# Performance work log

Measured on AMD Instinct MI355X. Metric: run time of the kernel, lower is better.

The kernel has to match this reference:

```python
import jax, jax.numpy as jnp
import numpy as np

VOCAB = 10000
HID = 256
BATCH = 32
STEPS = 256


def setup_inputs() -> dict:
    key = jax.random.key(0)
    ks = jax.random.split(key, 8)
    X = jax.random.randint(ks[0], (BATCH, STEPS), 0, VOCAB)
    H = jnp.zeros((BATCH, HID), dtype=jnp.float32)
    s = 0.01
    inp = {
        "X": X,
        "H": H,
        "W_xz": jax.random.normal(ks[1], (VOCAB, HID), jnp.float32) * s,
        "W_hz": jax.random.normal(ks[2], (HID, HID), jnp.float32) * s,
        "b_z": jnp.zeros((HID,), jnp.float32),
        "W_xr": jax.random.normal(ks[3], (VOCAB, HID), jnp.float32) * s,
        "W_hr": jax.random.normal(ks[4], (HID, HID), jnp.float32) * s,
        "b_r": jnp.zeros((HID,), jnp.float32),
        "W_xh": jax.random.normal(ks[5], (VOCAB, HID), jnp.float32) * s,
        "W_hh": jax.random.normal(ks[6], (HID, HID), jnp.float32) * s,
        "b_h": jnp.zeros((HID,), jnp.float32),
        "W_hq": jax.random.normal(ks[7], (HID, VOCAB), jnp.float32) * s,
        "b_q": jnp.zeros((VOCAB,), jnp.float32),
    }
    return inp


def reference(X, H, W_xz, W_hz, b_z, W_xr, W_hr, b_r, W_xh, W_hh, b_h, W_hq, b_q):
    # one-hot of X.T -> (steps, batch, vocab) float32
    Xo = jax.nn.one_hot(X.T, VOCAB, dtype=jnp.float32)

    def step(h, x):  # x: (batch, vocab), h: (batch, hid)
        z = jax.nn.sigmoid(x @ W_xz + h @ W_hz + b_z)
        r = jax.nn.sigmoid(x @ W_xr + h @ W_hr + b_r)
        h_tilda = jnp.tanh(x @ W_xh + (r * h) @ W_hh + b_h)
        h_new = z * h + (1.0 - z) * h_tilda
        y = h_new @ W_hq + b_q  # (batch, vocab)
        return h_new, y

    H_final, Ys = jax.lax.scan(step, H, Xo)
    out = Ys.reshape(STEPS * BATCH, VOCAB)  # matches torch.cat(outputs, dim=0)
    return out, (H_final,)
```

## Files before the change

### kernel.cpp

```cpp
#include <hip/hip_runtime.h>
#include <hip/hip_bf16.h>
#include <stdint.h>

#define VOCAB 10000
#define HID   256
#define BATCH 32
#define STEPS 256

typedef __attribute__((ext_vector_type(8))) short short8;
typedef __attribute__((ext_vector_type(4))) float floatx4;

__device__ __forceinline__ float bf2f(unsigned short u) {
    union { unsigned int ui; float f; } v;
    v.ui = ((unsigned int)u) << 16;
    return v.f;
}

__device__ __forceinline__ unsigned short f2bf(float f) {
    union { float f; unsigned int ui; } v;
    v.f = f;
    unsigned int u = v.ui;
    unsigned int r = (u + 0x7FFFu + ((u >> 16) & 1u)) >> 16;
    return (unsigned short)r;
}

#if __has_builtin(__builtin_amdgcn_fdot2_f32_bf16)
typedef __bf16 bf16x2 __attribute__((ext_vector_type(2)));
__device__ __forceinline__ float dot2(unsigned int w, unsigned int h, float acc) {
    union { unsigned int u; bf16x2 v; } a, b;
    a.u = w; b.u = h;
    return __builtin_amdgcn_fdot2_f32_bf16(a.v, b.v, acc, false);
}
#else
__device__ __forceinline__ float dot2(unsigned int w, unsigned int h, float acc) {
    union { unsigned int u; float f; } w0, w1, h0, h1;
    w0.u = w << 16; w1.u = w & 0xFFFF0000u;
    h0.u = h << 16; h1.u = h & 0xFFFF0000u;
    acc = fmaf(w0.f, h0.f, acc);
    acc = fmaf(w1.f, h1.f, acc);
    return acc;
}
#endif

__device__ __forceinline__ float sigmoidf_(float x) {
    return __builtin_amdgcn_rcpf(1.0f + __expf(-x));
}
__device__ __forceinline__ float tanhf_(float x) {
    float e = __expf(2.0f * x);
    return 1.0f - 2.0f * __builtin_amdgcn_rcpf(e + 1.0f);
}

__global__ void prep_w(const float* __restrict__ Wz, const float* __restrict__ Wr,
                       const float* __restrict__ Wh, unsigned short* __restrict__ out) {
    int g = blockIdx.x, k = blockIdx.y, j = threadIdx.x;
    const float* W = (g == 0) ? Wz : (g == 1) ? Wr : Wh;
    float v = W[k * HID + j];
    int p4 = k >> 3, m = k & 7;
    out[(((size_t)g * 32 + p4) * HID + j) * 8 + m] = f2bf(v);
}

__global__ void prep_b(const float* __restrict__ Whq, unsigned short* __restrict__ bfr) {
    int k = blockIdx.y;
    int n = blockIdx.x * 256 + threadIdx.x;
    if (n >= VOCAB) return;
    float v = Whq[(size_t)k * VOCAB + n];
    int nt = n >> 4, l15 = n & 15;
    int kc = k >> 5, kr = k & 31;
    int quad = kr >> 3, jj = kr & 7;
    int lane = quad * 16 + l15;
    bfr[(((size_t)nt * 8 + kc) * 64 + lane) * 8 + jj] = f2bf(v);
}

__global__ __launch_bounds__(512, 1) void gru_rec(
    const int* __restrict__ X, const float* __restrict__ H0,
    const float* __restrict__ Wxz, const float* __restrict__ Wxr,
    const float* __restrict__ Wxh,
    const float* __restrict__ bz, const float* __restrict__ br,
    const float* __restrict__ bh,
    const unsigned short* __restrict__ Wsw,
    unsigned short* __restrict__ hist,
    float* __restrict__ h_final)
{
    const int b = blockIdx.x;
    const int tid = threadIdx.x;
    const bool isA = tid < HID;
    const int j = isA ? tid : tid - HID;

    __shared__ __align__(16) unsigned short hbuf[HID];
    __shared__ __align__(16) unsigned short rhbuf[HID];
    __shared__ float part[HID];
    __shared__ float xrow[2][3][HID];
    __shared__ int Xl[STEPS];

    const uint4* wA = (const uint4*)Wsw + (size_t)(isA ? 0 : 1) * 32 * HID + j;
    const uint4* wH = (const uint4*)Wsw + (size_t)2 * 32 * HID + j;

    float h_my = H0[b * HID + j];
    float bias = isA ? bz[j] : br[j];
    float bhj  = isA ? bh[j] : 0.0f;

    uint4 wreg[32];
    #pragma unroll
    for (int i = 0; i < 32; ++i) wreg[i] = wA[i * HID];

    const int i0 = isA ? 0 : 16;
    uint4 whreg[16];
    #pragma unroll
    for (int i = 0; i < 16; ++i) whreg[i] = wH[(i0 + i) * HID];

    if (isA) { hbuf[j] = f2bf(h_my); Xl[j] = X[b * STEPS + j]; }
    __syncthreads();

    {
        int x0 = Xl[0];
        if (isA) {
            xrow[0][0][j] = Wxz[(size_t)x0 * HID + j];
            xrow[0][2][j] = Wxh[(size_t)x0 * HID + j];
        } else {
            xrow[0][1][j] = Wxr[(size_t)x0 * HID + j];
        }
    }
    __syncthreads();

    float z = 0.0f;

    for (int t = 0; t < STEPS; ++t) {
        const int cur = t & 1, nxt = cur ^ 1;

        const int xn = Xl[(t + 1) & (STEPS - 1)];
        float p0 = 0.f, p1 = 0.f;
        if (isA) {
            p0 = Wxz[(size_t)xn * HID + j];
            p1 = Wxh[(size_t)xn * HID + j];
        } else {
            p0 = Wxr[(size_t)xn * HID + j];
        }

        float acc;
        {
            const uint4* hp = (const uint4*)hbuf;
            float a0 = 0.f, a1 = 0.f, a2 = 0.f, a3 = 0.f;
            #pragma unroll
            for (int i = 0; i < 32; ++i) {
                uint4 hv = hp[i];
                a0 = dot2(wreg[i].x, hv.x, a0);
                a1 = dot2(wreg[i].y, hv.y, a1);
                a2 = dot2(wreg[i].z, hv.z, a2);
                a3 = dot2(wreg[i].w, hv.w, a3);
            }
            acc = (a0 + a1) + (a2 + a3);
        }

        if (isA) {
            z = sigmoidf_(acc + xrow[cur][0][j] + bias);
            xrow[nxt][0][j] = p0;
            xrow[nxt][2][j] = p1;
        } else {
            float r = sigmoidf_(acc + xrow[cur][1][j] + bias);
            rhbuf[j] = f2bf(r * h_my);
            xrow[nxt][1][j] = p0;
        }
        __syncthreads();

        float acch;
        {
            const uint4* rp = (const uint4*)rhbuf;
            float a0 = 0.f, a1 = 0.f, a2 = 0.f, a3 = 0.f;
            #pragma unroll
            for (int i = 0; i < 16; ++i) {
                uint4 hv = rp[i0 + i];
                a0 = dot2(whreg[i].x, hv.x, a0);
                a1 = dot2(whreg[i].y, hv.y, a1);
                a2 = dot2(whreg[i].z, hv.z, a2);
                a3 = dot2(whreg[i].w, hv.w, a3);
            }
            acch = (a0 + a1) + (a2 + a3);
        }
        if (!isA) part[j] = acch;
        __syncthreads();

        if (isA) {
            float hpre = acch + part[j] + xrow[cur][2][j] + bhj;
            float ht = tanhf_(hpre);
            float hn = z * h_my + (1.0f - z) * ht;
            h_my = hn;
            unsigned short hb = f2bf(hn);
            hbuf[j] = hb;
            hist[((size_t)t * BATCH + b) * HID + j] = hb;
        }
        __syncthreads();

        if (!isA) h_my = bf2f(hbuf[j]);
    }

    if (isA) h_final[b * HID + j] = h_my;
}

__global__ __launch_bounds__(256, 2) void proj(
    const unsigned short* __restrict__ Abf,
    const unsigned short* __restrict__ Bfr,
    const float* __restrict__ bq,
    float* __restrict__ C)
{
    const int tid  = threadIdx.x;
    const int wave = tid >> 6;
    const int lane = tid & 63;
    const int l15  = lane & 15;
    const int quad = lane >> 4;

    const int nb = blockIdx.x;
    const int mb = blockIdx.y;
    const int m0 = mb * 128;
    const int nt0 = nb * 16 + wave * 4;

    floatx4 acc[8][4];
    #pragma unroll
    for (int i = 0; i < 8; ++i)
        #pragma unroll
        for (int q = 0; q < 4; ++q)
            acc[i][q] = (floatx4)0.0f;

    int ntc[4];
    #pragma unroll
    for (int q = 0; q < 4; ++q) {
        int nt = nt0 + q;
        ntc[q] = (nt < 625) ? nt : 624;
    }

    for (int kc = 0; kc < 8; ++kc) {
        short8 a[8];
        #pragma unroll
        for (int mt = 0; mt < 8; ++mt) {
            const unsigned short* ap =
                Abf + (size_t)(m0 + mt * 16 + l15) * HID + kc * 32 + quad * 8;
            a[mt] = *(const short8*)ap;
        }
        short8 bfrg[4];
        #pragma unroll
        for (int q = 0; q < 4; ++q) {
            const unsigned short* bp =
                Bfr + ((((size_t)ntc[q] * 8 + kc) * 64) + lane) * 8;
            bfrg[q] = *(const short8*)bp;
        }
        #pragma unroll
        for (int mt = 0; mt < 8; ++mt)
            #pragma unroll
            for (int q = 0; q < 4; ++q)
                acc[mt][q] = __builtin_amdgcn_mfma_f32_16x16x32_bf16(
                    a[mt], bfrg[q], acc[mt][q], 0, 0, 0);
    }

    #pragma unroll
    for (int q = 0; q < 4; ++q) {
        int nt = nt0 + q;
        if (nt >= 625) continue;
        int col = nt * 16 + l15;
        float bqv = bq[col];
        #pragma unroll
        for (int mt = 0; mt < 8; ++mt) {
            int rowb = m0 + mt * 16 + quad * 4;
            #pragma unroll
            for (int r = 0; r < 4; ++r) {
                C[(size_t)(rowb + r) * VOCAB + col] = acc[mt][q][r] + bqv;
            }
        }
    }
}

extern "C" void kernel_launch(void* const* d_in, const int* in_sizes, int n_in,
                              void* d_out, int out_size, void* d_ws, size_t ws_size,
                              hipStream_t stream) {
    const int*   X   = (const int*)  d_in[0];
    const float* H0  = (const float*)d_in[1];
    const float* Wxz = (const float*)d_in[2];
    const float* Whz = (const float*)d_in[3];
    const float* bz  = (const float*)d_in[4];
    const float* Wxr = (const float*)d_in[5];
    const float* Whr = (const float*)d_in[6];
    const float* br  = (const float*)d_in[7];
    const float* Wxh = (const float*)d_in[8];
    const float* Whh = (const float*)d_in[9];
    const float* bh  = (const float*)d_in[10];
    const float* Whq = (const float*)d_in[11];
    const float* bq  = (const float*)d_in[12];

    float* out     = (float*)d_out;
    float* h_final = out + (size_t)STEPS * BATCH * VOCAB;

    unsigned short* wsw  = (unsigned short*)d_ws;
    unsigned short* bfr  = wsw + 196608;
    unsigned short* hist = bfr + 2560000;

    prep_w<<<dim3(3, 256), 256, 0, stream>>>(Whz, Whr, Whh, wsw);
    prep_b<<<dim3(40, 256), 256, 0, stream>>>(Whq, bfr);
    gru_rec<<<BATCH, 512, 0, stream>>>(X, H0, Wxz, Wxr, Wxh, bz, br, bh,
                                       wsw, hist, h_final);
    proj<<<dim3(40, 64), 256, 0, stream>>>(hist, bfr, bq, out);
}
```

Measured before the change: 851.2 us.

## Vectorize weight prep and projection stores, remap proj blocks per XCD

The weight-prep kernels now pack eight bf16 values per thread and store them as one 16-byte write. prep_b stages a tile of W_hq through LDS to get a transposed layout, so global reads and writes are both coalesced. The projection swaps the MFMA operand order so each lane holds four consecutive output columns and can write 16-byte float4 stores with a float4 bias load. Blocks are also remapped so each XCD handles a contiguous group of N-tiles, which should improve L2 reuse of the B fragments. These changes target the store-bound 82 MB output write and the scattered 2-byte prep stores, at the cost of more complex indexing.

```diff
diff --git a/kernel.cpp b/kernel.cpp
--- a/kernel.cpp
+++ b/kernel.cpp
@@ -52,23 +52,44 @@
 
 __global__ void prep_w(const float* __restrict__ Wz, const float* __restrict__ Wr,
                        const float* __restrict__ Wh, unsigned short* __restrict__ out) {
-    int g = blockIdx.x, k = blockIdx.y, j = threadIdx.x;
+    int g = blockIdx.x, p4 = blockIdx.y, j = threadIdx.x;
     const float* W = (g == 0) ? Wz : (g == 1) ? Wr : Wh;
-    float v = W[k * HID + j];
-    int p4 = k >> 3, m = k & 7;
-    out[(((size_t)g * 32 + p4) * HID + j) * 8 + m] = f2bf(v);
+    union { unsigned short us[8]; short8 v; } pk;
+    #pragma unroll
+    for (int m = 0; m < 8; ++m)
+        pk.us[m] = f2bf(W[(p4 * 8 + m) * HID + j]);
+    *(short8*)(out + (((size_t)g * 32 + p4) * HID + j) * 8) = pk.v;
 }
 
 __global__ void prep_b(const float* __restrict__ Whq, unsigned short* __restrict__ bfr) {
-    int k = blockIdx.y;
-    int n = blockIdx.x * 256 + threadIdx.x;
-    if (n >= VOCAB) return;
-    float v = Whq[(size_t)k * VOCAB + n];
-    int nt = n >> 4, l15 = n & 15;
-    int kc = k >> 5, kr = k & 31;
-    int quad = kr >> 3, jj = kr & 7;
-    int lane = quad * 16 + l15;
-    bfr[(((size_t)nt * 8 + kc) * 64 + lane) * 8 + jj] = f2bf(v);
+    __shared__ float lds[32][257];
+    const int nb = blockIdx.x;
+    const int kc = blockIdx.y;
+    const int tid = threadIdx.x;
+    const int n0 = nb * 256;
+
+    #pragma unroll 4
+    for (int kk = 0; kk < 32; ++kk) {
+        int n = n0 + tid;
+        float v = (n < VOCAB) ? Whq[(size_t)(kc * 32 + kk) * VOCAB + n] : 0.0f;
+        lds[kk][tid] = v;
+    }
+    __syncthreads();
+
+    const int lane = tid & 63;
+    const int wq   = tid >> 6;
+    const int quad = lane >> 4, l15 = lane & 15;
+    #pragma unroll
+    for (int ntp = 0; ntp < 4; ++ntp) {
+        int nt_local = ntp * 4 + wq;
+        int nt = nb * 16 + nt_local;
+        if (nt >= 625) continue;
+        union { unsigned short us[8]; short8 v; } pk;
+        #pragma unroll
+        for (int jj = 0; jj < 8; ++jj)
+            pk.us[jj] = f2bf(lds[quad * 8 + jj][nt_local * 16 + l15]);
+        *(short8*)(bfr + (((size_t)nt * 8 + kc) * 64 + lane) * 8) = pk.v;
+    }
 }
 
 __global__ __launch_bounds__(512, 1) void gru_rec(
@@ -208,8 +229,12 @@
     const int l15  = lane & 15;
     const int quad = lane >> 4;
 
-    const int nb = blockIdx.x;
-    const int mb = blockIdx.y;
+    const int orig = blockIdx.x;
+    const int xcd  = orig & 7;
+    const int idx  = orig >> 3;
+    const int mb   = idx / 5;
+    const int nb   = xcd * 5 + (idx % 5);
+
     const int m0 = mb * 128;
     const int nt0 = nb * 16 + wave * 4;
 
@@ -247,22 +272,25 @@
             #pragma unroll
             for (int q = 0; q < 4; ++q)
                 acc[mt][q] = __builtin_amdgcn_mfma_f32_16x16x32_bf16(
-                    a[mt], bfrg[q], acc[mt][q], 0, 0, 0);
-    }
-
+                    bfrg[q], a[mt], acc[mt][q], 0, 0, 0);
+    }
+
+    floatx4 bq4[4];
     #pragma unroll
     for (int q = 0; q < 4; ++q) {
         int nt = nt0 + q;
-        if (nt >= 625) continue;
-        int col = nt * 16 + l15;
-        float bqv = bq[col];
-        #pragma unroll
-        for (int mt = 0; mt < 8; ++mt) {
-            int rowb = m0 + mt * 16 + quad * 4;
-            #pragma unroll
-            for (int r = 0; r < 4; ++r) {
-                C[(size_t)(rowb + r) * VOCAB + col] = acc[mt][q][r] + bqv;
-            }
+        bq4[q] = (nt < 625) ? *(const floatx4*)(bq + nt * 16 + quad * 4)
+                            : (floatx4)0.0f;
+    }
+    #pragma unroll
+    for (int mt = 0; mt < 8; ++mt) {
+        const size_t rowoff = (size_t)(m0 + mt * 16 + l15) * VOCAB;
+        #pragma unroll
+        for (int q = 0; q < 4; ++q) {
+            int nt = nt0 + q;
+            if (nt >= 625) continue;
+            floatx4 v = acc[mt][q] + bq4[q];
+            *(floatx4*)(C + rowoff + nt * 16 + quad * 4) = v;
         }
     }
 }
@@ -291,9 +319,9 @@
     unsigned short* bfr  = wsw + 196608;
     unsigned short* hist = bfr + 2560000;
 
-    prep_w<<<dim3(3, 256), 256, 0, stream>>>(Whz, Whr, Whh, wsw);
-    prep_b<<<dim3(40, 256), 256, 0, stream>>>(Whq, bfr);
+    prep_w<<<dim3(3, 32), 256, 0, stream>>>(Whz, Whr, Whh, wsw);
+    prep_b<<<dim3(40, 8), 256, 0, stream>>>(Whq, bfr);
     gru_rec<<<BATCH, 512, 0, stream>>>(X, H0, Wxz, Wxr, Wxh, bz, br, bh,
                                        wsw, hist, h_final);
-    proj<<<dim3(40, 64), 256, 0, stream>>>(hist, bfr, bq, out);
-}
+    proj<<<2560, 256, 0, stream>>>(hist, bfr, bq, out);
+}
```

Result: faster. 827.3 us (-2.8%).
